# Kernel optimization log

Measured on AMD Instinct MI355X. Metric: run time of the kernel, lower is better.

## Reference

```python
import jax, jax.numpy as jnp
import numpy as np

N_NODES = 30000
N_EDGES = 300000
NUM_GRAPHS = 512
HID = 600
IN_FEATS = 9
NUM_TASKS = 128


def setup_inputs() -> dict:
    key = jax.random.key(0)
    ks = jax.random.split(key, 20)
    s = 0.05  # small init scale to keep activations bounded over 5 layers
    inp = {
        'x': jax.random.normal(ks[0], (N_NODES, IN_FEATS), jnp.float32),
        'edge_index': jax.random.randint(ks[1], (2, N_EDGES), 0, N_NODES, jnp.int64),
        'batch_ind': jnp.sort(jax.random.randint(ks[2], (N_NODES,), 0, NUM_GRAPHS, jnp.int64)),
        'w1_0': jax.random.normal(ks[3], (IN_FEATS, HID), jnp.float32) * s,
        'b1_0': jax.random.normal(ks[4], (HID,), jnp.float32) * s,
        'w2_0': jax.random.normal(ks[5], (HID, HID), jnp.float32) * s,
        'b2_0': jax.random.normal(ks[6], (HID,), jnp.float32) * s,
        'w1_r': jax.random.normal(ks[7], (4, HID, HID), jnp.float32) * s,
        'b1_r': jax.random.normal(ks[8], (4, HID), jnp.float32) * s,
        'w2_r': jax.random.normal(ks[9], (4, HID, HID), jnp.float32) * s,
        'b2_r': jax.random.normal(ks[10], (4, HID), jnp.float32) * s,
        'cw1': jax.random.normal(ks[11], (HID, 256), jnp.float32) * s,
        'cb1': jax.random.normal(ks[12], (256,), jnp.float32) * s,
        'cw2': jax.random.normal(ks[13], (256, 256), jnp.float32) * s,
        'cb2': jax.random.normal(ks[14], (256,), jnp.float32) * s,
        'cw3': jax.random.normal(ks[15], (256, NUM_TASKS), jnp.float32) * s,
        'cb3': jax.random.normal(ks[16], (NUM_TASKS,), jnp.float32) * s,
    }
    return inp


def _gin_conv(h, edge_index, w1, b1, w2, b2):
    # sum-aggregate neighbor features: messages flow src -> dst
    msgs = h[edge_index[0]]                                   # [E, d] gather
    agg = jax.ops.segment_sum(msgs, edge_index[1], num_segments=N_NODES)
    z = h + agg                                               # (1 + eps) * x + agg, eps = 0
    z = jax.nn.relu(z @ w1 + b1) @ w2 + b2                    # per-layer MLP [in, 600, 600]
    return z


def _forward(x, edge_index, batch_ind, w1_0, b1_0, w2_0, b2_0,
             w1_r, b1_r, w2_r, b2_r, cw1, cb1, cw2, cb2, cw3, cb3):
    h = _gin_conv(x, edge_index, w1_0, b1_0, w2_0, b2_0)
    h = jax.nn.relu(h)  # inter-layer activation (dropout is identity in eval)
    for i in range(4):  # layers 1..4 (fixed, structurally distinct params)
        h = _gin_conv(h, edge_index, w1_r[i], b1_r[i], w2_r[i], b2_r[i])
        if i < 3:
            h = jax.nn.relu(h)  # no act/dropout after final GNN layer (jk=None)
    feats = jax.ops.segment_sum(h, batch_ind, num_segments=NUM_GRAPHS)  # global_add_pool
    z = jax.nn.relu(feats @ cw1 + cb1)
    z = jax.nn.relu(z @ cw2 + cb2)
    return z @ cw3 + cb3  # [NUM_GRAPHS, NUM_TASKS]


def reference(x, edge_index, batch_ind, w1_0, b1_0, w2_0, b2_0,
              w1_r, b1_r, w2_r, b2_r, cw1, cb1, cw2, cb2, cw3, cb3):
    return _forward(x, edge_index, batch_ind, w1_0, b1_0, w2_0, b2_0,
                    w1_r, b1_r, w2_r, b2_r, cw1, cb1, cw2, cb2, cw3, cb3)
```

## Files before the change

### kernel.cpp

```cpp
#include <hip/hip_runtime.h>

#define N_NODES 30000
#define N_EDGES 300000
#define NUM_GRAPHS 512
#define HID 600
#define IN_FEATS 9
#define NUM_TASKS 128

#define MPAD 30080
#define HPAD 640
#define K0PAD 32

typedef __attribute__((ext_vector_type(4))) float f32x4;
typedef __attribute__((ext_vector_type(8))) short bf16x8;


__device__ __forceinline__ float bflo(unsigned int v) {
  union { unsigned int u; float f; } c; c.u = v << 16; return c.f;
}
__device__ __forceinline__ float bfhi(unsigned int v) {
  union { unsigned int u; float f; } c; c.u = v & 0xffff0000u; return c.f;
}
__device__ __forceinline__ unsigned short f2bf(float f) {
  union { float f; unsigned int u; } c; c.f = f;
  unsigned int u = c.u;
  return (unsigned short)((u + 0x7fffu + ((u >> 16) & 1u)) >> 16);
}
__device__ __forceinline__ unsigned int pack2(float a, float b) {
  return (unsigned int)f2bf(a) | ((unsigned int)f2bf(b) << 16);
}


__global__ void k_hist(const int* __restrict__ keys, int* __restrict__ counts, int n) {
  int i = blockIdx.x * blockDim.x + threadIdx.x;
  if (i < n) atomicAdd(&counts[keys[i]], 1);
}

__global__ __launch_bounds__(1024) void k_exscan(const int* __restrict__ in,
                                                 int* __restrict__ out,
                                                 int* cursor, int n) {
  __shared__ int buf[1024];
  int tid = threadIdx.x;
  int CH = (n + 1023) / 1024;
  int base = tid * CH;
  int s = 0;
  for (int j = 0; j < CH; ++j) {
    int i = base + j;
    if (i < n) s += in[i];
  }
  buf[tid] = s;
  __syncthreads();
  for (int off = 1; off < 1024; off <<= 1) {
    int t = (tid >= off) ? buf[tid - off] : 0;
    __syncthreads();
    buf[tid] += t;
    __syncthreads();
  }
  int pre = (tid == 0) ? 0 : buf[tid - 1];
  for (int j = 0; j < CH; ++j) {
    int i = base + j;
    if (i <= n) out[i] = pre;
    if (i < n) {
      int v = in[i];
      if (cursor) cursor[i] = pre;
      pre += v;
    }
  }
}

__global__ __launch_bounds__(256) void k_scan1(const int* __restrict__ in,
                                               int* __restrict__ partials, int n) {
  __shared__ int buf[256];
  int i = blockIdx.x * 256 + threadIdx.x;
  buf[threadIdx.x] = (i < n) ? in[i] : 0;
  __syncthreads();
  for (int off = 128; off; off >>= 1) {
    if (threadIdx.x < off) buf[threadIdx.x] += buf[threadIdx.x + off];
    __syncthreads();
  }
  if (threadIdx.x == 0) partials[blockIdx.x] = buf[0];
}

__global__ __launch_bounds__(256) void k_scan3(const int* __restrict__ in,
                                               const int* __restrict__ poff,
                                               int* __restrict__ out,
                                               int* __restrict__ cursor, int n) {
  __shared__ int buf[256];
  int b = blockIdx.x, t = threadIdx.x;
  int i = b * 256 + t;
  int v = (i < n) ? in[i] : 0;
  buf[t] = v;
  __syncthreads();
  for (int off = 1; off < 256; off <<= 1) {
    int x = (t >= off) ? buf[t - off] : 0;
    __syncthreads();
    buf[t] += x;
    __syncthreads();
  }
  int base = poff[b];
  int excl = base + buf[t] - v;
  if (i < n) {
    out[i] = excl;
    cursor[i] = excl;
    if (i == n - 1) out[n] = base + buf[t];
  }
}

__global__ void k_scatter(const int* __restrict__ src, const int* __restrict__ dst,
                          int* __restrict__ cursor, int* __restrict__ edge_src, int E) {
  int e = blockIdx.x * blockDim.x + threadIdx.x;
  if (e < E) {
    int pos = atomicAdd(&cursor[dst[e]], 1);
    edge_src[pos] = src[e];
  }
}


__global__ void k_wt0(const float* __restrict__ w1_0, unsigned short* __restrict__ wt0) {
  int idx = blockIdx.x * 256 + threadIdx.x;
  if (idx >= HPAD * K0PAD) return;
  int n = idx / K0PAD, k = idx % K0PAD;
  float v = (n < HID && k < IN_FEATS) ? w1_0[(size_t)k * HID + n] : 0.f;
  wt0[idx] = f2bf(v);
}

__global__ __launch_bounds__(256) void k_wt_tiled(
    const float* __restrict__ w2_0, const float* __restrict__ w1_r,
    const float* __restrict__ w2_r, unsigned short* __restrict__ wts) {
  __shared__ float tile[64][65];
  int b = blockIdx.x;
  int w = b / 100;
  int tb = b % 100;
  int tn = (tb % 10) * 64;
  int tk = (tb / 10) * 64;
  const float* W;
  if (w == 0) W = w2_0;
  else if (w < 5) W = w1_r + (size_t)(w - 1) * HID * HID;
  else W = w2_r + (size_t)(w - 5) * HID * HID;
  int t = threadIdx.x;
  int lx = t & 63, ly = t >> 6;
#pragma unroll
  for (int i = 0; i < 16; ++i) {
    int k = tk + ly + i * 4;
    int n = tn + lx;
    float v = (k < HID && n < HID) ? W[(size_t)k * HID + n] : 0.f;
    tile[ly + i * 4][lx] = v;
  }
  __syncthreads();
  unsigned short* dst = wts + (size_t)w * HPAD * HPAD;
#pragma unroll
  for (int i = 0; i < 16; ++i) {
    int n = tn + ly + i * 4;
    int k = tk + lx;
    dst[(size_t)n * HPAD + k] = f2bf(tile[lx][ly + i * 4]);
  }
}

__global__ void k_bias_all(const float* __restrict__ b1_0, const float* __restrict__ b2_0,
                           const float* __restrict__ b1_r, const float* __restrict__ b2_r,
                           float* __restrict__ biases) {
  int idx = blockIdx.x * 256 + threadIdx.x;
  if (idx >= 10 * HPAD) return;
  int w = idx / HPAD, i = idx % HPAD;
  float v = 0.f;
  if (i < HID) {
    if (w == 0) v = b1_0[i];
    else if (w == 1) v = b2_0[i];
    else if (w < 6) v = b1_r[(size_t)(w - 2) * HID + i];
    else v = b2_r[(size_t)(w - 6) * HID + i];
  }
  biases[idx] = v;
}

__global__ void k_xconv(const float* __restrict__ x, unsigned short* __restrict__ xb) {
  int idx = blockIdx.x * 256 + threadIdx.x;
  if (idx >= MPAD * K0PAD) return;
  int m = idx >> 5, k = idx & 31;
  float v = (m < N_NODES && k < IN_FEATS) ? x[(size_t)m * IN_FEATS + k] : 0.f;
  xb[idx] = f2bf(v);
}


template <int U>
__global__ __launch_bounds__(256) void k_agg_bf16(
    const unsigned int* __restrict__ h, const int* __restrict__ ptr,
    const int* __restrict__ esrc, unsigned int* __restrict__ z, int n_nodes) {
  int wave = threadIdx.x >> 6, lane = threadIdx.x & 63;
  int node = blockIdx.x * 4 + wave;
  if (node >= n_nodes) return;
  int beg = ptr[node], end = ptr[node + 1];
  const unsigned int* hn = h + (size_t)node * U;
  float a0[5], a1[5];
#pragma unroll
  for (int i = 0; i < 5; ++i) {
    int u = lane + i * 64;
    if (u < U) { unsigned int v = hn[u]; a0[i] = bflo(v); a1[i] = bfhi(v); }
    else { a0[i] = 0.f; a1[i] = 0.f; }
  }
  int e = beg;
  for (; e + 4 <= end; e += 4) {
    const unsigned int* p0 = h + (size_t)esrc[e] * U;
    const unsigned int* p1 = h + (size_t)esrc[e + 1] * U;
    const unsigned int* p2 = h + (size_t)esrc[e + 2] * U;
    const unsigned int* p3 = h + (size_t)esrc[e + 3] * U;
    unsigned int v0[5], v1[5], v2[5], v3[5];
#pragma unroll
    for (int i = 0; i < 5; ++i) {
      int u = lane + i * 64;
      if (u < U) { v0[i] = p0[u]; v1[i] = p1[u]; v2[i] = p2[u]; v3[i] = p3[u]; }
      else { v0[i] = 0; v1[i] = 0; v2[i] = 0; v3[i] = 0; }
    }
#pragma unroll
    for (int i = 0; i < 5; ++i) {
      a0[i] += (bflo(v0[i]) + bflo(v1[i])) + (bflo(v2[i]) + bflo(v3[i]));
      a1[i] += (bfhi(v0[i]) + bfhi(v1[i])) + (bfhi(v2[i]) + bfhi(v3[i]));
    }
  }
  for (; e < end; ++e) {
    const unsigned int* p0 = h + (size_t)esrc[e] * U;
#pragma unroll
    for (int i = 0; i < 5; ++i) {
      int u = lane + i * 64;
      if (u < U) { unsigned int v = p0[u]; a0[i] += bflo(v); a1[i] += bfhi(v); }
    }
  }
  unsigned int* zn = z + (size_t)node * U;
#pragma unroll
  for (int i = 0; i < 5; ++i) {
    int u = lane + i * 64;
    if (u < U) zn[u] = pack2(a0[i], a1[i]);
  }
}


__global__ __launch_bounds__(256) void k_pool_bf16(
    const unsigned int* __restrict__ h, const int* __restrict__ gptr,
    float* __restrict__ feats) {
  const int U = HPAD / 2;
  __shared__ float red[4][HPAD];
  int t = threadIdx.x;
  int wave = t >> 6, lane = t & 63;
  int g = blockIdx.x;
  int beg = gptr[g], end = gptr[g + 1];
  float a0[5] = {0.f, 0.f, 0.f, 0.f, 0.f}, a1[5] = {0.f, 0.f, 0.f, 0.f, 0.f};
  for (int i = beg + wave; i < end; i += 4) {
    const unsigned int* hi = h + (size_t)i * U;
#pragma unroll
    for (int j = 0; j < 5; ++j) {
      unsigned int v = hi[lane + j * 64];
      a0[j] += bflo(v); a1[j] += bfhi(v);
    }
  }
#pragma unroll
  for (int j = 0; j < 5; ++j) {
    int u = lane + j * 64;
    red[wave][2 * u] = a0[j];
    red[wave][2 * u + 1] = a1[j];
  }
  __syncthreads();
  float* fg = feats + (size_t)g * HPAD;
  for (int c = t; c < HPAD; c += 256)
    fg[c] = red[0][c] + red[1][c] + red[2][c] + red[3][c];
}


#define GLOAD(gptr, lptr)                                                            \
  __builtin_amdgcn_global_load_lds(                                                  \
      (const __attribute__((address_space(1))) unsigned int*)(gptr),                 \
      (__attribute__((address_space(3))) unsigned int*)(lptr), 16, 0, 0)

__global__ __launch_bounds__(256) void k_mgemm(
    const unsigned short* __restrict__ A, const unsigned short* __restrict__ Bt,
    const float* __restrict__ bias, unsigned short* __restrict__ C,
    int lda, int ldb, int ldc, int K, int relu, int gy) {
  int G = gridDim.x;
  int orig = blockIdx.x;
  int q = G >> 3, r = G & 7;
  int xcd = orig & 7, local = orig >> 3;
  int wgid = (xcd < r ? xcd * (q + 1) : r * (q + 1) + (xcd - r) * q) + local;
  int n0 = (wgid % gy) * 128;
  int m0 = (wgid / gy) * 128;

  __shared__ unsigned short As[3][128 * 32];
  __shared__ unsigned short Bs[3][128 * 32];
  int t = threadIdx.x;
  int lane = t & 63, wave = t >> 6;
  int wm = (wave >> 1) * 64, wn = (wave & 1) * 64;

  f32x4 acc[4][4] = {};

  int off0 = t * 8, off1 = t * 8 + 2048;
  int rm0 = off0 >> 5, rk0 = off0 & 31;
  int rm1 = off1 >> 5, rk1 = off1 & 31;

  const unsigned short* Ar0 = A + (size_t)(m0 + rm0) * lda + rk0;
  const unsigned short* Ar1 = A + (size_t)(m0 + rm1) * lda + rk1;
  const unsigned short* Br0 = Bt + (size_t)(n0 + rm0) * ldb + rk0;
  const unsigned short* Br1 = Bt + (size_t)(n0 + rm1) * ldb + rk1;

  int nt = K >> 5;
  GLOAD(Ar0, &As[0][off0]);
  GLOAD(Ar1, &As[0][off1]);
  GLOAD(Br0, &Bs[0][off0]);
  GLOAD(Br1, &Bs[0][off1]);
  if (nt > 1) {
    GLOAD(Ar0 + 32, &As[1][off0]);
    GLOAD(Ar1 + 32, &As[1][off1]);
    GLOAD(Br0 + 32, &Bs[1][off0]);
    GLOAD(Br1 + 32, &Bs[1][off1]);
  }

  int kk = (lane >> 4) * 8;
  int ra = wm + (lane & 15);
  int rb = wn + (lane & 15);
  int cur = 0;

  for (int tt = 0; tt < nt; ++tt) {
    if (tt + 1 < nt) {
      asm volatile("s_waitcnt vmcnt(4)" ::: "memory");
    } else {
      asm volatile("s_waitcnt vmcnt(0)" ::: "memory");
    }
    __builtin_amdgcn_s_barrier();
    if (tt + 2 < nt) {
      int k2 = (tt + 2) << 5;
      int nb = cur + 2; if (nb >= 3) nb -= 3;
      GLOAD(Ar0 + k2, &As[nb][off0]);
      GLOAD(Ar1 + k2, &As[nb][off1]);
      GLOAD(Br0 + k2, &Bs[nb][off0]);
      GLOAD(Br1 + k2, &Bs[nb][off1]);
    }
    bf16x8 a[4], b[4];
#pragma unroll
    for (int i = 0; i < 4; ++i)
      a[i] = *(const bf16x8*)(&As[cur][(ra + i * 16) * 32 + kk]);
#pragma unroll
    for (int j = 0; j < 4; ++j)
      b[j] = *(const bf16x8*)(&Bs[cur][(rb + j * 16) * 32 + kk]);
#pragma unroll
    for (int i = 0; i < 4; ++i)
#pragma unroll
      for (int j = 0; j < 4; ++j)
        acc[i][j] = __builtin_amdgcn_mfma_f32_16x16x32_bf16(b[j], a[i], acc[i][j], 0, 0, 0);
    cur += 1; if (cur >= 3) cur = 0;
  }

  int colm = lane & 15;
  int nq = (lane >> 4) * 4;
#pragma unroll
  for (int j = 0; j < 4; ++j) {
    int n = n0 + wn + j * 16 + nq;
    f32x4 bv = *(const f32x4*)&bias[n];
#pragma unroll
    for (int i = 0; i < 4; ++i) {
      int m = m0 + wm + i * 16 + colm;
      float v0 = acc[i][j][0] + bv[0];
      float v1 = acc[i][j][1] + bv[1];
      float v2 = acc[i][j][2] + bv[2];
      float v3 = acc[i][j][3] + bv[3];
      if (relu) {
        v0 = fmaxf(v0, 0.f); v1 = fmaxf(v1, 0.f);
        v2 = fmaxf(v2, 0.f); v3 = fmaxf(v3, 0.f);
      }
      uint2 w;
      w.x = pack2(v0, v1);
      w.y = pack2(v2, v3);
      *(uint2*)&C[(size_t)m * ldc + n] = w;
    }
  }
}


__global__ __launch_bounds__(256) void k_classifier(
    const float* __restrict__ feats,
    const float* __restrict__ cw1, const float* __restrict__ cb1,
    const float* __restrict__ cw2, const float* __restrict__ cb2,
    const float* __restrict__ cw3, const float* __restrict__ cb3,
    float* __restrict__ out) {
  __shared__ float f[HID];
  __shared__ float red[4][256];
  __shared__ float z1[256];
  __shared__ float z2[256];
  int g = blockIdx.x;
  int t = threadIdx.x;
  int wave = t >> 6, lane = t & 63;
  for (int i = t; i < HID; i += 256) f[i] = feats[(size_t)g * HPAD + i];
  __syncthreads();

  {
    float acc[4] = {0.f, 0.f, 0.f, 0.f};
    int k0 = wave * 150, k1 = k0 + 150;
    for (int k = k0; k < k1; ++k) {
      float fv = f[k];
      const float* row = cw1 + (size_t)k * 256;
#pragma unroll
      for (int j = 0; j < 4; ++j) acc[j] += fv * row[lane + j * 64];
    }
#pragma unroll
    for (int j = 0; j < 4; ++j) red[wave][lane + j * 64] = acc[j];
  }
  __syncthreads();
  z1[t] = fmaxf(red[0][t] + red[1][t] + red[2][t] + red[3][t] + cb1[t], 0.f);
  __syncthreads();

  {
    float acc[4] = {0.f, 0.f, 0.f, 0.f};
    int k0 = wave * 64, k1 = k0 + 64;
    for (int k = k0; k < k1; ++k) {
      float zv = z1[k];
      const float* row = cw2 + (size_t)k * 256;
#pragma unroll
      for (int j = 0; j < 4; ++j) acc[j] += zv * row[lane + j * 64];
    }
    __syncthreads();
#pragma unroll
    for (int j = 0; j < 4; ++j) red[wave][lane + j * 64] = acc[j];
  }
  __syncthreads();
  z2[t] = fmaxf(red[0][t] + red[1][t] + red[2][t] + red[3][t] + cb2[t], 0.f);
  __syncthreads();

  {
    float a0 = 0.f, a1 = 0.f;
    int k0 = wave * 64, k1 = k0 + 64;
    for (int k = k0; k < k1; ++k) {
      float zv = z2[k];
      const float* row = cw3 + (size_t)k * NUM_TASKS;
      a0 += zv * row[lane];
      a1 += zv * row[lane + 64];
    }
    __syncthreads();
    red[wave][lane] = a0;
    red[wave][lane + 64] = a1;
  }
  __syncthreads();
  if (t < NUM_TASKS)
    out[(size_t)g * NUM_TASKS + t] = red[0][t] + red[1][t] + red[2][t] + red[3][t] + cb3[t];
}


extern "C" void kernel_launch(void* const* d_in, const int* in_sizes, int n_in,
                              void* d_out, int out_size, void* d_ws, size_t ws_size,
                              hipStream_t stream) {
  const float* x      = (const float*)d_in[0];
  const int*   ei     = (const int*)d_in[1];
  const int*   batch  = (const int*)d_in[2];
  const float* w1_0   = (const float*)d_in[3];
  const float* b1_0   = (const float*)d_in[4];
  const float* w2_0   = (const float*)d_in[5];
  const float* b2_0   = (const float*)d_in[6];
  const float* w1_r   = (const float*)d_in[7];
  const float* b1_r   = (const float*)d_in[8];
  const float* w2_r   = (const float*)d_in[9];
  const float* b2_r   = (const float*)d_in[10];
  const float* cw1    = (const float*)d_in[11];
  const float* cb1    = (const float*)d_in[12];
  const float* cw2    = (const float*)d_in[13];
  const float* cb2    = (const float*)d_in[14];
  const float* cw3    = (const float*)d_in[15];
  const float* cb3    = (const float*)d_in[16];
  float* out = (float*)d_out;

  const int* e_src = ei;
  const int* e_dst = ei + N_EDGES;

  const size_t HBUF = (size_t)MPAD * HPAD;
  const size_t ZBUF = (size_t)MPAD * K0PAD;
  const size_t WT   = (size_t)HPAD * HPAD;
  const int NB = (N_NODES + 255) / 256;

  unsigned short* hA  = (unsigned short*)d_ws;
  unsigned short* hB  = hA + HBUF;
  unsigned short* hC  = hB + HBUF;
  unsigned short* z0  = hC + HBUF;
  unsigned short* xb  = z0 + ZBUF;
  unsigned short* wt0 = xb + ZBUF;
  unsigned short* wts = wt0 + (size_t)HPAD * K0PAD;
  float* biases = (float*)(wts + 9 * WT);
  float* feats  = biases + 10 * HPAD;
  int* row_ptr  = (int*)(feats + (size_t)NUM_GRAPHS * HPAD);
  int* counts   = row_ptr + (N_NODES + 1);
  int* edge_src = counts + N_NODES;
  int* gptr     = edge_src + N_EDGES;
  int* gcnt     = gptr + (NUM_GRAPHS + 1);
  int* partials = gcnt + NUM_GRAPHS;
  int* poff     = partials + (NB + 1);

  k_wt0<<<(HPAD * K0PAD + 255) / 256, 256, 0, stream>>>(w1_0, wt0);
  k_wt_tiled<<<9 * 100, 256, 0, stream>>>(w2_0, w1_r, w2_r, wts);
  k_bias_all<<<(10 * HPAD + 255) / 256, 256, 0, stream>>>(b1_0, b2_0, b1_r, b2_r, biases);
  k_xconv<<<(MPAD * K0PAD + 255) / 256, 256, 0, stream>>>(x, xb);

  hipMemsetAsync(counts, 0, N_NODES * sizeof(int), stream);
  k_hist<<<(N_EDGES + 255) / 256, 256, 0, stream>>>(e_dst, counts, N_EDGES);
  k_scan1<<<NB, 256, 0, stream>>>(counts, partials, N_NODES);
  k_exscan<<<1, 1024, 0, stream>>>(partials, poff, nullptr, NB);
  k_scan3<<<NB, 256, 0, stream>>>(counts, poff, row_ptr, counts, N_NODES);
  k_scatter<<<(N_EDGES + 255) / 256, 256, 0, stream>>>(e_src, e_dst, counts, edge_src, N_EDGES);

  hipMemsetAsync(gcnt, 0, NUM_GRAPHS * sizeof(int), stream);
  k_hist<<<(N_NODES + 255) / 256, 256, 0, stream>>>(batch, gcnt, N_NODES);
  k_exscan<<<1, 1024, 0, stream>>>(gcnt, gptr, nullptr, NUM_GRAPHS);

  const int G = (MPAD / 128) * (HPAD / 128);
  const int GY = HPAD / 128;

  k_agg_bf16<K0PAD / 2><<<(N_NODES + 3) / 4, 256, 0, stream>>>(
      (const unsigned int*)xb, row_ptr, edge_src, (unsigned int*)z0, N_NODES);
  k_mgemm<<<G, 256, 0, stream>>>(z0, wt0, biases + 0 * HPAD, hC, K0PAD, K0PAD, HPAD, K0PAD, 1, GY);
  k_mgemm<<<G, 256, 0, stream>>>(hC, wts, biases + 1 * HPAD, hA, HPAD, HPAD, HPAD, HPAD, 1, GY);

  unsigned short* h = hA;
  unsigned short* z = hB;
  unsigned short* tb = hC;
  for (int i = 0; i < 4; ++i) {
    k_agg_bf16<HPAD / 2><<<(N_NODES + 3) / 4, 256, 0, stream>>>(
        (const unsigned int*)h, row_ptr, edge_src, (unsigned int*)z, N_NODES);
    k_mgemm<<<G, 256, 0, stream>>>(z, wts + (1 + (size_t)i) * WT, biases + (2 + i) * HPAD, tb,
                                   HPAD, HPAD, HPAD, HPAD, 1, GY);
    k_mgemm<<<G, 256, 0, stream>>>(tb, wts + (5 + (size_t)i) * WT, biases + (6 + i) * HPAD, z,
                                   HPAD, HPAD, HPAD, HPAD, (i < 3) ? 1 : 0, GY);
    unsigned short* tmp = h; h = z; z = tmp;
  }

  k_pool_bf16<<<NUM_GRAPHS, 256, 0, stream>>>((const unsigned int*)h, gptr, feats);
  k_classifier<<<NUM_GRAPHS, 256, 0, stream>>>(feats, cw1, cb1, cw2, cb2, cw3, cb3, out);
}
```

Baseline: 798.6 us.

## Use 512-thread GEMM blocks and stage epilogue through swizzled LDS

The bf16 MFMA GEMM now runs 8 waves per 128x128 tile, each computing a 64x32 sub-tile, so each thread issues one global-to-LDS load per operand per k-step instead of two. This halves per-wave accumulators and raises the wave count per CU. The epilogue writes packed results into an XOR-swizzled shared buffer and then does coalesced 16-byte row stores to global memory, replacing scattered 8-byte stores. The cost is two extra barriers and LDS traffic, and each wave gets less MFMA work per LDS fragment load.

```diff
diff --git a/kernel.cpp b/kernel.cpp
--- a/kernel.cpp
+++ b/kernel.cpp
@@ -269,7 +269,7 @@
       (const __attribute__((address_space(1))) unsigned int*)(gptr),                 \
       (__attribute__((address_space(3))) unsigned int*)(lptr), 16, 0, 0)
 
-__global__ __launch_bounds__(256) void k_mgemm(
+__global__ __launch_bounds__(512, 6) void k_mgemm(
     const unsigned short* __restrict__ A, const unsigned short* __restrict__ Bt,
     const float* __restrict__ bias, unsigned short* __restrict__ C,
     int lda, int ldb, int ldc, int K, int relu, int gy) {
@@ -281,33 +281,29 @@
   int n0 = (wgid % gy) * 128;
   int m0 = (wgid / gy) * 128;
 
-  __shared__ unsigned short As[3][128 * 32];
-  __shared__ unsigned short Bs[3][128 * 32];
+  __shared__ unsigned short smem[3 * 4096 * 2];
+  unsigned short* Asb = smem;
+  unsigned short* Bsb = smem + 12288;
+
   int t = threadIdx.x;
   int lane = t & 63, wave = t >> 6;
-  int wm = (wave >> 1) * 64, wn = (wave & 1) * 64;
-
-  f32x4 acc[4][4] = {};
-
-  int off0 = t * 8, off1 = t * 8 + 2048;
-  int rm0 = off0 >> 5, rk0 = off0 & 31;
-  int rm1 = off1 >> 5, rk1 = off1 & 31;
-
-  const unsigned short* Ar0 = A + (size_t)(m0 + rm0) * lda + rk0;
-  const unsigned short* Ar1 = A + (size_t)(m0 + rm1) * lda + rk1;
-  const unsigned short* Br0 = Bt + (size_t)(n0 + rm0) * ldb + rk0;
-  const unsigned short* Br1 = Bt + (size_t)(n0 + rm1) * ldb + rk1;
+  int wm = (wave >> 2) * 64;
+  int wn = (wave & 3) * 32;
+
+  f32x4 acc[4][2] = {};
+
+  int off = t * 8;
+  int rm = off >> 5, rk = off & 31;
+
+  const unsigned short* Ar = A + (size_t)(m0 + rm) * lda + rk;
+  const unsigned short* Br = Bt + (size_t)(n0 + rm) * ldb + rk;
 
   int nt = K >> 5;
-  GLOAD(Ar0, &As[0][off0]);
-  GLOAD(Ar1, &As[0][off1]);
-  GLOAD(Br0, &Bs[0][off0]);
-  GLOAD(Br1, &Bs[0][off1]);
+  GLOAD(Ar, Asb + off);
+  GLOAD(Br, Bsb + off);
   if (nt > 1) {
-    GLOAD(Ar0 + 32, &As[1][off0]);
-    GLOAD(Ar1 + 32, &As[1][off1]);
-    GLOAD(Br0 + 32, &Bs[1][off0]);
-    GLOAD(Br1 + 32, &Bs[1][off1]);
+    GLOAD(Ar + 32, Asb + 4096 + off);
+    GLOAD(Br + 32, Bsb + 4096 + off);
   }
 
   int kk = (lane >> 4) * 8;
@@ -317,7 +313,7 @@
 
   for (int tt = 0; tt < nt; ++tt) {
     if (tt + 1 < nt) {
-      asm volatile("s_waitcnt vmcnt(4)" ::: "memory");
+      asm volatile("s_waitcnt vmcnt(2)" ::: "memory");
     } else {
       asm volatile("s_waitcnt vmcnt(0)" ::: "memory");
     }
@@ -325,35 +321,34 @@
     if (tt + 2 < nt) {
       int k2 = (tt + 2) << 5;
       int nb = cur + 2; if (nb >= 3) nb -= 3;
-      GLOAD(Ar0 + k2, &As[nb][off0]);
-      GLOAD(Ar1 + k2, &As[nb][off1]);
-      GLOAD(Br0 + k2, &Bs[nb][off0]);
-      GLOAD(Br1 + k2, &Bs[nb][off1]);
-    }
-    bf16x8 a[4], b[4];
+      GLOAD(Ar + k2, Asb + nb * 4096 + off);
+      GLOAD(Br + k2, Bsb + nb * 4096 + off);
+    }
+    bf16x8 a[4], b[2];
 #pragma unroll
     for (int i = 0; i < 4; ++i)
-      a[i] = *(const bf16x8*)(&As[cur][(ra + i * 16) * 32 + kk]);
-#pragma unroll
-    for (int j = 0; j < 4; ++j)
-      b[j] = *(const bf16x8*)(&Bs[cur][(rb + j * 16) * 32 + kk]);
+      a[i] = *(const bf16x8*)(Asb + cur * 4096 + (ra + i * 16) * 32 + kk);
+#pragma unroll
+    for (int j = 0; j < 2; ++j)
+      b[j] = *(const bf16x8*)(Bsb + cur * 4096 + (rb + j * 16) * 32 + kk);
 #pragma unroll
     for (int i = 0; i < 4; ++i)
 #pragma unroll
-      for (int j = 0; j < 4; ++j)
+      for (int j = 0; j < 2; ++j)
         acc[i][j] = __builtin_amdgcn_mfma_f32_16x16x32_bf16(b[j], a[i], acc[i][j], 0, 0, 0);
     cur += 1; if (cur >= 3) cur = 0;
   }
 
+  __syncthreads();
   int colm = lane & 15;
   int nq = (lane >> 4) * 4;
 #pragma unroll
-  for (int j = 0; j < 4; ++j) {
-    int n = n0 + wn + j * 16 + nq;
-    f32x4 bv = *(const f32x4*)&bias[n];
+  for (int j = 0; j < 2; ++j) {
+    int nloc = wn + j * 16 + nq;
+    f32x4 bv = *(const f32x4*)&bias[n0 + nloc];
 #pragma unroll
     for (int i = 0; i < 4; ++i) {
-      int m = m0 + wm + i * 16 + colm;
+      int mloc = wm + i * 16 + colm;
       float v0 = acc[i][j][0] + bv[0];
       float v1 = acc[i][j][1] + bv[1];
       float v2 = acc[i][j][2] + bv[2];
@@ -365,8 +360,24 @@
       uint2 w;
       w.x = pack2(v0, v1);
       w.y = pack2(v2, v3);
-      *(uint2*)&C[(size_t)m * ldc + n] = w;
-    }
+      int nblk = (nloc >> 2) ^ ((mloc & 7) << 2);
+      *(uint2*)&smem[mloc * 128 + nblk * 4] = w;
+    }
+  }
+  __syncthreads();
+#pragma unroll
+  for (int p = 0; p < 4; ++p) {
+    int idx = p * 4096 + t * 8;
+    int mloc = idx >> 7;
+    int ncol = idx & 127;
+    int s = (mloc & 7) << 2;
+    int nb0 = (ncol >> 2) ^ s;
+    int nb1 = ((ncol >> 2) + 1) ^ s;
+    uint2 w0 = *(uint2*)&smem[mloc * 128 + nb0 * 4];
+    uint2 w1 = *(uint2*)&smem[mloc * 128 + nb1 * 4];
+    uint4 w;
+    w.x = w0.x; w.y = w0.y; w.z = w1.x; w.w = w1.y;
+    *(uint4*)&C[(size_t)(m0 + mloc) * ldc + n0 + ncol] = w;
   }
 }
 
@@ -507,8 +518,8 @@
 
   k_agg_bf16<K0PAD / 2><<<(N_NODES + 3) / 4, 256, 0, stream>>>(
       (const unsigned int*)xb, row_ptr, edge_src, (unsigned int*)z0, N_NODES);
-  k_mgemm<<<G, 256, 0, stream>>>(z0, wt0, biases + 0 * HPAD, hC, K0PAD, K0PAD, HPAD, K0PAD, 1, GY);
-  k_mgemm<<<G, 256, 0, stream>>>(hC, wts, biases + 1 * HPAD, hA, HPAD, HPAD, HPAD, HPAD, 1, GY);
+  k_mgemm<<<G, 512, 0, stream>>>(z0, wt0, biases + 0 * HPAD, hC, K0PAD, K0PAD, HPAD, K0PAD, 1, GY);
+  k_mgemm<<<G, 512, 0, stream>>>(hC, wts, biases + 1 * HPAD, hA, HPAD, HPAD, HPAD, HPAD, 1, GY);
 
   unsigned short* h = hA;
   unsigned short* z = hB;
@@ -516,9 +527,9 @@
   for (int i = 0; i < 4; ++i) {
     k_agg_bf16<HPAD / 2><<<(N_NODES + 3) / 4, 256, 0, stream>>>(
         (const unsigned int*)h, row_ptr, edge_src, (unsigned int*)z, N_NODES);
-    k_mgemm<<<G, 256, 0, stream>>>(z, wts + (1 + (size_t)i) * WT, biases + (2 + i) * HPAD, tb,
+    k_mgemm<<<G, 512, 0, stream>>>(z, wts + (1 + (size_t)i) * WT, biases + (2 + i) * HPAD, tb,
                                    HPAD, HPAD, HPAD, HPAD, 1, GY);
-    k_mgemm<<<G, 256, 0, stream>>>(tb, wts + (5 + (size_t)i) * WT, biases + (6 + i) * HPAD, z,
+    k_mgemm<<<G, 512, 0, stream>>>(tb, wts + (5 + (size_t)i) * WT, biases + (6 + i) * HPAD, z,
                                    HPAD, HPAD, HPAD, HPAD, (i < 3) ? 1 : 0, GY);
     unsigned short* tmp = h; h = z; z = tmp;
   }
```

Measured after the change: 720.9 us. -9.7%, faster.
